# Kernel tuning notes

Hardware: AMD Instinct MI355X
Metric: run time of the kernel (lower is better)

The kernel has to match this reference:

```python
import jax, jax.numpy as jnp
import numpy as np

B, T, C, HD = 4, 4096, 1024, 64  # batch, seq, n_embd, head_dim = n_embd//n_head


def setup_inputs() -> dict:
    key = jax.random.key(0)
    k1, k2, k3, k4 = jax.random.split(key, 4)
    scale = 0.02
    return {
        "x": jax.random.normal(k1, (B, T, C), dtype=jnp.float32),
        "Wq": jax.random.normal(k2, (C, HD), dtype=jnp.float32) * scale,
        "Wk": jax.random.normal(k3, (C, HD), dtype=jnp.float32) * scale,
        "Wv": jax.random.normal(k4, (C, HD), dtype=jnp.float32) * scale,
    }


def reference(x, Wq, Wk, Wv):
    # single-head projections: [B,T,C] @ [C,HD] -> [B,T,HD]
    q = jnp.einsum("btc,ch->bth", x, Wq)
    k = jnp.einsum("btc,ch->bth", x, Wk)
    v = jnp.einsum("btc,ch->bth", x, Wv)
    scale = k.shape[-1] ** -0.5
    # scores: [B,T,T], causal mask via -inf, stable softmax
    alpha = jnp.einsum("bqh,bkh->bqk", q, k) * scale
    t = x.shape[1]
    causal = jnp.tril(jnp.ones((t, t), dtype=bool))
    alpha = jnp.where(causal, alpha, -jnp.inf)
    alpha = jax.nn.softmax(alpha, axis=-1)
    # dropout p=0.0 -> identity
    h = jnp.einsum("bqk,bkh->bqh", alpha, v)
    return h
```

## Files before the change

kernel.cpp:

```cpp
#include <hip/hip_runtime.h>

#define T_SEQ 4096
#define C_DIM 1024
#define HD 64
#define NCH 272

typedef __attribute__((ext_vector_type(8))) __bf16 bf16x8;
typedef __attribute__((ext_vector_type(8))) unsigned short us8;
typedef __attribute__((ext_vector_type(4))) unsigned short us4;
typedef __attribute__((ext_vector_type(4))) float f32x4;
typedef __attribute__((ext_vector_type(16))) float f32x16;

#define QSCALE 0.18033688011112042f

__device__ __forceinline__ unsigned short f2bf(float f) {
    union { float f; unsigned u; } x; x.f = f;
    unsigned r = x.u + 0x7FFFu + ((x.u >> 16) & 1u);
    return (unsigned short)(r >> 16);
}

__device__ __forceinline__ float bf2f(unsigned short u) {
    union { unsigned u; float f; } x; x.u = ((unsigned)u) << 16;
    return x.f;
}

__device__ __forceinline__ us8 cvt8(float4 a, float4 b) {
    union { __bf16 h[8]; us8 v; } u;
    u.h[0] = (__bf16)a.x; u.h[1] = (__bf16)a.y; u.h[2] = (__bf16)a.z; u.h[3] = (__bf16)a.w;
    u.h[4] = (__bf16)b.x; u.h[5] = (__bf16)b.y; u.h[6] = (__bf16)b.z; u.h[7] = (__bf16)b.w;
    return u.v;
}

__device__ __forceinline__ us4 cvt4f(float a, float b, float c, float d) {
    union { __bf16 h[4]; us4 v; } u;
    u.h[0] = (__bf16)a; u.h[1] = (__bf16)b; u.h[2] = (__bf16)c; u.h[3] = (__bf16)d;
    return u.v;
}

__device__ __forceinline__ f32x16 zero16() {
    f32x16 v;
    #pragma unroll
    for (int j = 0; j < 16; ++j) v[j] = 0.f;
    return v;
}

__device__ __forceinline__ int swzs(int idx) {
    return idx ^ ((((idx) >> 6) & 7) << 3);
}

__device__ __forceinline__ int offf(int qt) {
    const int m = qt >> 1;
    return (qt & 1) ? (m + 1) * (m + 1) : m * m + m;
}

__global__ __launch_bounds__(256) void k_wtrans(const float* __restrict__ Wq,
                                                const float* __restrict__ Wk,
                                                const float* __restrict__ Wv,
                                                unsigned short* __restrict__ wt_g) {
    __shared__ unsigned short tile[64][72];
    const int bx = blockIdx.x;
    const int which = bx >> 4;
    const int k0 = (bx & 15) * 64;
    const float* W = (which == 0) ? Wq : ((which == 1) ? Wk : Wv);
    const int t = threadIdx.x;
    {
        const int r = t >> 2, c0 = (t & 3) * 16;
        const float4* src = reinterpret_cast<const float4*>(W + (k0 + r) * HD + c0);
        #pragma unroll
        for (int i = 0; i < 4; ++i) {
            float4 v = src[i];
            tile[r][c0 + 4 * i + 0] = f2bf(v.x);
            tile[r][c0 + 4 * i + 1] = f2bf(v.y);
            tile[r][c0 + 4 * i + 2] = f2bf(v.z);
            tile[r][c0 + 4 * i + 3] = f2bf(v.w);
        }
    }
    __syncthreads();
    {
        const int n = t >> 2, kc0 = (t & 3) * 16;
        alignas(16) unsigned short o[16];
        #pragma unroll
        for (int i = 0; i < 16; ++i) o[i] = tile[kc0 + i][n];
        unsigned short* dst = wt_g + (size_t)(which * 64 + n) * 1024 + k0 + kc0;
        *reinterpret_cast<us8*>(dst)     = *reinterpret_cast<const us8*>(&o[0]);
        *reinterpret_cast<us8*>(dst + 8) = *reinterpret_cast<const us8*>(&o[8]);
    }
}

__global__ __launch_bounds__(256) void k_proj(const float* __restrict__ x,
                                              const unsigned short* __restrict__ wt_g,
                                              unsigned short* __restrict__ qs,
                                              unsigned short* __restrict__ ksb,
                                              unsigned short* __restrict__ vt) {
    __shared__ unsigned short smem[6656];
    unsigned short* xs0 = smem;
    unsigned short* xs1 = smem + 2304;
    const int tid = threadIdx.x;
    const int w = tid >> 6, lane = tid & 63;
    const int l15 = lane & 15, g = lane >> 4;
    const int m0 = blockIdx.x * 32;
    const int sr = tid >> 3, sc0 = (tid & 7) * 8;
    const float* xrow = x + (size_t)(m0 + sr) * C_DIM + sc0;
    const unsigned short* wrow[3];
    #pragma unroll
    for (int mf = 0; mf < 3; ++mf)
        wrow[mf] = wt_g + (size_t)((3 * w + mf) * 16 + l15) * C_DIM + g * 8;

    f32x4 acc[3][2];
    #pragma unroll
    for (int mf = 0; mf < 3; ++mf)
        #pragma unroll
        for (int nf = 0; nf < 2; ++nf)
            acc[mf][nf] = (f32x4){0.f, 0.f, 0.f, 0.f};

    {
        float4 xa = *reinterpret_cast<const float4*>(xrow);
        float4 xb = *reinterpret_cast<const float4*>(xrow + 4);
        *reinterpret_cast<us8*>(xs0 + sr * 72 + sc0) = cvt8(xa, xb);
    }
    float4 p1a = *reinterpret_cast<const float4*>(xrow + 64);
    float4 p1b = *reinterpret_cast<const float4*>(xrow + 68);
    us8 wc[3][2];
    #pragma unroll
    for (int mf = 0; mf < 3; ++mf)
        #pragma unroll
        for (int k2 = 0; k2 < 2; ++k2)
            wc[mf][k2] = *reinterpret_cast<const us8*>(wrow[mf] + k2 * 32);
    __syncthreads();

    for (int kk = 0; kk < 16; ++kk) {
        unsigned short* xcur = (kk & 1) ? xs1 : xs0;
        unsigned short* xnxt = (kk & 1) ? xs0 : xs1;
        float4 p2a, p2b;
        us8 wn[3][2];
        if (kk < 14) {
            p2a = *reinterpret_cast<const float4*>(xrow + (kk + 2) * 64);
            p2b = *reinterpret_cast<const float4*>(xrow + (kk + 2) * 64 + 4);
        }
        if (kk < 15) {
            #pragma unroll
            for (int mf = 0; mf < 3; ++mf)
                #pragma unroll
                for (int k2 = 0; k2 < 2; ++k2)
                    wn[mf][k2] = *reinterpret_cast<const us8*>(wrow[mf] + (kk + 1) * 64 + k2 * 32);
        }
        #pragma unroll
        for (int k2 = 0; k2 < 2; ++k2) {
            bf16x8 bfr[2];
            #pragma unroll
            for (int nf = 0; nf < 2; ++nf)
                bfr[nf] = *reinterpret_cast<const bf16x8*>(xcur + (nf * 16 + l15) * 72 + k2 * 32 + g * 8);
            #pragma unroll
            for (int mf = 0; mf < 3; ++mf) {
                bf16x8 afr = *reinterpret_cast<const bf16x8*>(&wc[mf][k2]);
                #pragma unroll
                for (int nf = 0; nf < 2; ++nf)
                    acc[mf][nf] = __builtin_amdgcn_mfma_f32_16x16x32_bf16(
                        afr, bfr[nf], acc[mf][nf], 0, 0, 0);
            }
        }
        if (kk < 15) {
            *reinterpret_cast<us8*>(xnxt + sr * 72 + sc0) = cvt8(p1a, p1b);
            #pragma unroll
            for (int mf = 0; mf < 3; ++mf)
                #pragma unroll
                for (int k2 = 0; k2 < 2; ++k2)
                    wc[mf][k2] = wn[mf][k2];
        }
        p1a = p2a; p1b = p2b;
        __syncthreads();
    }

    unsigned short* out_lds = smem;
    #pragma unroll
    for (int mf = 0; mf < 3; ++mf) {
        const int Mfr = 3 * w + mf;
        const float s = (Mfr < 4) ? QSCALE : 1.0f;
        #pragma unroll
        for (int nf = 0; nf < 2; ++nf) {
            union { __bf16 h[4]; us4 v; } u;
            #pragma unroll
            for (int r = 0; r < 4; ++r) u.h[r] = (__bf16)(acc[mf][nf][r] * s);
            *reinterpret_cast<us4*>(out_lds + (nf * 16 + l15) * 208 + Mfr * 16 + 4 * g) = u.v;
        }
    }
    __syncthreads();
    {
        const int r = tid >> 3, c = (tid & 7) * 8;
        const size_t gm = (size_t)(m0 + r);
        *reinterpret_cast<us8*>(qs + gm * 64 + c)  = *reinterpret_cast<const us8*>(out_lds + r * 208 + c);
        *reinterpret_cast<us8*>(ksb + gm * 64 + c) = *reinterpret_cast<const us8*>(out_lds + r * 208 + 64 + c);
    }
    {
        const int d = tid >> 2, j0 = (tid & 3) * 8;
        const int b = m0 >> 12, t0 = m0 & 4095;
        alignas(16) unsigned short tmp[8];
        #pragma unroll
        for (int j = 0; j < 8; ++j) tmp[j] = out_lds[(j0 + j) * 208 + 128 + d];
        *reinterpret_cast<us8*>(vt + (size_t)(b * 64 + d) * T_SEQ + t0 + j0) =
            *reinterpret_cast<const us8*>(tmp);
    }
}

__global__ __launch_bounds__(256) void k_attn(const unsigned short* __restrict__ qs,
                                              const unsigned short* __restrict__ ks,
                                              const unsigned short* __restrict__ vt,
                                              unsigned short* __restrict__ Opart,
                                              float* __restrict__ lw,
                                              float* __restrict__ out) {
    __shared__ unsigned short sm[16384];
    const int tid = threadIdx.x;
    const int w = tid >> 6, lane = tid & 63;
    const int l31 = lane & 31, hi = lane >> 5;
    const int batch = blockIdx.y;
    const int i = (NCH - 1) - blockIdx.x;
    int qt = min(31, (int)(2.0f * sqrtf((float)i)));
    while (offf(qt + 1) <= i) ++qt;
    while (offf(qt) > i) --qt;
    const int s = i - offf(qt);
    const int ns = (qt + 2) >> 1;
    const int it0 = s * 4;
    const int it1 = min(it0 + 4, 2 * qt + 2);
    const int qi = qt * 128 + 32 * w + l31;
    const size_t qrow = (size_t)batch * T_SEQ + qi;

    bf16x8 qf[4];
    #pragma unroll
    for (int df = 0; df < 4; ++df)
        qf[df] = *reinterpret_cast<const bf16x8*>(qs + qrow * 64 + df * 16 + hi * 8);

    f32x16 accO0 = zero16(), accO1 = zero16();
    float l_run = 0.f;

    const int sr = tid >> 2, sc0 = (tid & 3) * 16;
    const unsigned short* kbase = ks + ((size_t)batch * T_SEQ + sr) * 64 + sc0;
    const unsigned short* vbase = vt + ((size_t)batch * 64 + sr) * T_SEQ + sc0;

    {
        us8 a0 = *reinterpret_cast<const us8*>(kbase + (size_t)it0 * 4096);
        us8 a1 = *reinterpret_cast<const us8*>(kbase + (size_t)it0 * 4096 + 8);
        us8 b0 = *reinterpret_cast<const us8*>(vbase + it0 * 64);
        us8 b1 = *reinterpret_cast<const us8*>(vbase + it0 * 64 + 8);
        us8 w0, w1;
        #pragma unroll
        for (int j = 0; j < 4; ++j) { w0[j] = b0[j]; w0[4 + j] = b1[j]; w1[j] = b0[4 + j]; w1[4 + j] = b1[4 + j]; }
        const int kd = sr * 64 + sc0, vd = 8192 + sr * 64 + sc0;
        *reinterpret_cast<us8*>(sm + swzs(kd))     = a0;
        *reinterpret_cast<us8*>(sm + swzs(kd + 8)) = a1;
        *reinterpret_cast<us8*>(sm + swzs(vd))     = w0;
        *reinterpret_cast<us8*>(sm + swzs(vd + 8)) = w1;
    }
    __syncthreads();

    for (int it = it0; it < it1; ++it) {
        const int cur = (it - it0) & 1;
        const bool pf = (it + 1 < it1);
        us8 n0, n1, m0, m1;
        if (pf) {
            n0 = *reinterpret_cast<const us8*>(kbase + (size_t)(it + 1) * 4096);
            n1 = *reinterpret_cast<const us8*>(kbase + (size_t)(it + 1) * 4096 + 8);
            m0 = *reinterpret_cast<const us8*>(vbase + (it + 1) * 64);
            m1 = *reinterpret_cast<const us8*>(vbase + (it + 1) * 64 + 8);
        }
        const int kb = cur * 4096;
        const int vb = 8192 + cur * 4096;
        const bool diag = (it >= 2 * qt);

        #pragma unroll
        for (int ksub = 0; ksub < 2; ++ksub) {
            f32x16 sv = zero16();
            __builtin_amdgcn_s_setprio(1);
            #pragma unroll
            for (int df = 0; df < 4; ++df) {
                bf16x8 afr = *reinterpret_cast<const bf16x8*>(
                    sm + swzs(kb + (ksub * 32 + l31) * 64 + df * 16 + hi * 8));
                sv = __builtin_amdgcn_mfma_f32_32x32x16_bf16(afr, qf[df], sv, 0, 0, 0);
            }
            __builtin_amdgcn_s_setprio(0);
            if (diag) {
                #pragma unroll
                for (int rr = 0; rr < 16; ++rr) {
                    const int kidx = it * 64 + ksub * 32 + (rr & 3) + 8 * (rr >> 2) + 4 * hi;
                    if (kidx > qi) sv[rr] = -1e30f;
                }
            }
            f32x16 pv;
            #pragma unroll
            for (int rr = 0; rr < 16; ++rr) {
                const float p = exp2f(sv[rr]);
                l_run += p;
                pv[rr] = p;
            }
            us8 bfr0, bfr1;
            {
                us4 c0 = cvt4f(pv[0], pv[1], pv[2], pv[3]);
                us4 c1 = cvt4f(pv[4], pv[5], pv[6], pv[7]);
                us4 c2 = cvt4f(pv[8], pv[9], pv[10], pv[11]);
                us4 c3 = cvt4f(pv[12], pv[13], pv[14], pv[15]);
                #pragma unroll
                for (int j = 0; j < 4; ++j) {
                    bfr0[j] = c0[j]; bfr0[4 + j] = c1[j];
                    bfr1[j] = c2[j]; bfr1[4 + j] = c3[j];
                }
            }
            __builtin_amdgcn_s_setprio(1);
            {
                bf16x8 a00 = *reinterpret_cast<const bf16x8*>(
                    sm + swzs(vb + l31 * 64 + ksub * 32 + hi * 8));
                bf16x8 a01 = *reinterpret_cast<const bf16x8*>(
                    sm + swzs(vb + l31 * 64 + ksub * 32 + 16 + hi * 8));
                accO0 = __builtin_amdgcn_mfma_f32_32x32x16_bf16(
                    a00, *reinterpret_cast<bf16x8*>(&bfr0), accO0, 0, 0, 0);
                accO0 = __builtin_amdgcn_mfma_f32_32x32x16_bf16(
                    a01, *reinterpret_cast<bf16x8*>(&bfr1), accO0, 0, 0, 0);
                bf16x8 a10 = *reinterpret_cast<const bf16x8*>(
                    sm + swzs(vb + (32 + l31) * 64 + ksub * 32 + hi * 8));
                bf16x8 a11 = *reinterpret_cast<const bf16x8*>(
                    sm + swzs(vb + (32 + l31) * 64 + ksub * 32 + 16 + hi * 8));
                accO1 = __builtin_amdgcn_mfma_f32_32x32x16_bf16(
                    a10, *reinterpret_cast<bf16x8*>(&bfr0), accO1, 0, 0, 0);
                accO1 = __builtin_amdgcn_mfma_f32_32x32x16_bf16(
                    a11, *reinterpret_cast<bf16x8*>(&bfr1), accO1, 0, 0, 0);
            }
            __builtin_amdgcn_s_setprio(0);
        }
        if (pf) {
            us8 w0, w1;
            #pragma unroll
            for (int j = 0; j < 4; ++j) { w0[j] = m0[j]; w0[4 + j] = m1[j]; w1[j] = m0[4 + j]; w1[4 + j] = m1[4 + j]; }
            const int kd = (cur ^ 1) * 4096 + sr * 64 + sc0;
            const int vd = 8192 + (cur ^ 1) * 4096 + sr * 64 + sc0;
            *reinterpret_cast<us8*>(sm + swzs(kd))     = n0;
            *reinterpret_cast<us8*>(sm + swzs(kd + 8)) = n1;
            *reinterpret_cast<us8*>(sm + swzs(vd))     = w0;
            *reinterpret_cast<us8*>(sm + swzs(vd + 8)) = w1;
        }
        __syncthreads();
    }

    l_run += __shfl_xor(l_run, 32, 64);

    if (ns == 1) {
        const float inv = 1.0f / l_run;
        #pragma unroll
        for (int rg = 0; rg < 4; ++rg) {
            const int d0 = 4 * hi + 8 * rg;
            f32x4 o0 = {accO0[4 * rg] * inv, accO0[4 * rg + 1] * inv,
                        accO0[4 * rg + 2] * inv, accO0[4 * rg + 3] * inv};
            f32x4 o1 = {accO1[4 * rg] * inv, accO1[4 * rg + 1] * inv,
                        accO1[4 * rg + 2] * inv, accO1[4 * rg + 3] * inv};
            *reinterpret_cast<f32x4*>(out + qrow * 64 + d0)      = o0;
            *reinterpret_cast<f32x4*>(out + qrow * 64 + 32 + d0) = o1;
        }
    } else {
        const int pb = batch * NCH + i;
        const int q = 32 * w + l31;
        unsigned short* ob = Opart + (size_t)pb * 8192 + q * 64;
        #pragma unroll
        for (int rg = 0; rg < 4; ++rg) {
            const int d0 = 4 * hi + 8 * rg;
            *reinterpret_cast<us4*>(ob + d0) =
                cvt4f(accO0[4 * rg], accO0[4 * rg + 1], accO0[4 * rg + 2], accO0[4 * rg + 3]);
            *reinterpret_cast<us4*>(ob + 32 + d0) =
                cvt4f(accO1[4 * rg], accO1[4 * rg + 1], accO1[4 * rg + 2], accO1[4 * rg + 3]);
        }
        if (hi == 0) lw[(size_t)pb * 128 + q] = l_run;
    }
}

__global__ __launch_bounds__(256) void k_combine(const unsigned short* __restrict__ Opart,
                                                 const float* __restrict__ lw,
                                                 float* __restrict__ out) {
    const int qt = 2 + (blockIdx.x >> 1), half = blockIdx.x & 1;
    const int batch = blockIdx.y;
    const int t = threadIdx.x;
    const int q = half * 64 + (t >> 2), d0 = (t & 3) * 16;
    const int ns = (qt + 2) >> 1;
    const int pb0 = batch * NCH + offf(qt);
    float num[16];
    #pragma unroll
    for (int j = 0; j < 16; ++j) num[j] = 0.f;
    float lsum = 0.f;
    for (int s = 0; s < ns; ++s) {
        const int pb = pb0 + s;
        lsum += lw[(size_t)pb * 128 + q];
        const unsigned short* op = Opart + (size_t)pb * 8192 + q * 64 + d0;
        us8 v0 = *reinterpret_cast<const us8*>(op);
        us8 v1 = *reinterpret_cast<const us8*>(op + 8);
        #pragma unroll
        for (int j = 0; j < 8; ++j) {
            num[j] += bf2f(v0[j]);
            num[8 + j] += bf2f(v1[j]);
        }
    }
    const float inv = 1.f / lsum;
    float* o = out + ((size_t)batch * T_SEQ + qt * 128 + q) * 64 + d0;
    #pragma unroll
    for (int h = 0; h < 4; ++h) {
        f32x4 v = {num[4 * h] * inv, num[4 * h + 1] * inv,
                   num[4 * h + 2] * inv, num[4 * h + 3] * inv};
        *reinterpret_cast<f32x4*>(o + 4 * h) = v;
    }
}

extern "C" void kernel_launch(void* const* d_in, const int* in_sizes, int n_in,
                              void* d_out, int out_size, void* d_ws, size_t ws_size,
                              hipStream_t stream) {
    (void)in_sizes; (void)n_in; (void)out_size; (void)ws_size;
    const float* x  = (const float*)d_in[0];
    const float* Wq = (const float*)d_in[1];
    const float* Wk = (const float*)d_in[2];
    const float* Wv = (const float*)d_in[3];
    float* out = (float*)d_out;
    unsigned short* ws16 = (unsigned short*)d_ws;
    unsigned short* wt_g  = ws16;
    unsigned short* qsb   = ws16 + 196608;
    unsigned short* ksb   = qsb + 1048576;
    unsigned short* vtb   = ksb + 1048576;
    unsigned short* Opart = vtb + 1048576;
    float* lw = (float*)(Opart + 8912896);
    k_wtrans <<<dim3(48),      dim3(256), 0, stream>>>(Wq, Wk, Wv, wt_g);
    k_proj   <<<dim3(512),     dim3(256), 0, stream>>>(x, wt_g, qsb, ksb, vtb);
    k_attn   <<<dim3(NCH, 4),  dim3(256), 0, stream>>>(qsb, ksb, vtb, Opart, lw, out);
    k_combine<<<dim3(60, 4),   dim3(256), 0, stream>>>(Opart, lw, out);
}
```

Baseline: 68.14 us.

## Stage x in 256-wide K groups and split softmax row-sum accumulator

The projection kernel now converts and stages x into LDS in 256-column groups, double-buffered across four outer iterations, instead of 64-column chunks. This cuts the number of block-wide barriers from sixteen to four and prefetches larger batches of global loads. It costs more LDS per block (about 33KB) and more registers for the eight prefetch float4s, which may lower occupancy. Separately, the attention kernel splits the running exp-sum into four independent accumulators to shorten the serial add dependency chain.

```diff
diff --git a/kernel.cpp b/kernel.cpp
--- a/kernel.cpp
+++ b/kernel.cpp
@@ -92,9 +92,7 @@
                                               unsigned short* __restrict__ qs,
                                               unsigned short* __restrict__ ksb,
                                               unsigned short* __restrict__ vt) {
-    __shared__ unsigned short smem[6656];
-    unsigned short* xs0 = smem;
-    unsigned short* xs1 = smem + 2304;
+    __shared__ unsigned short smem[16896];
     const int tid = threadIdx.x;
     const int w = tid >> 6, lane = tid & 63;
     const int l15 = lane & 15, g = lane >> 4;
@@ -113,13 +111,18 @@
         for (int nf = 0; nf < 2; ++nf)
             acc[mf][nf] = (f32x4){0.f, 0.f, 0.f, 0.f};
 
-    {
-        float4 xa = *reinterpret_cast<const float4*>(xrow);
-        float4 xb = *reinterpret_cast<const float4*>(xrow + 4);
-        *reinterpret_cast<us8*>(xs0 + sr * 72 + sc0) = cvt8(xa, xb);
-    }
-    float4 p1a = *reinterpret_cast<const float4*>(xrow + 64);
-    float4 p1b = *reinterpret_cast<const float4*>(xrow + 68);
+    #pragma unroll
+    for (int cg = 0; cg < 4; ++cg) {
+        float4 a = *reinterpret_cast<const float4*>(xrow + cg * 64);
+        float4 b = *reinterpret_cast<const float4*>(xrow + cg * 64 + 4);
+        *reinterpret_cast<us8*>(smem + sr * 264 + cg * 64 + sc0) = cvt8(a, b);
+    }
+    float4 pa[4], pb[4];
+    #pragma unroll
+    for (int cg = 0; cg < 4; ++cg) {
+        pa[cg] = *reinterpret_cast<const float4*>(xrow + 256 + cg * 64);
+        pb[cg] = *reinterpret_cast<const float4*>(xrow + 256 + cg * 64 + 4);
+    }
     us8 wc[3][2];
     #pragma unroll
     for (int mf = 0; mf < 3; ++mf)
@@ -128,46 +131,56 @@
             wc[mf][k2] = *reinterpret_cast<const us8*>(wrow[mf] + k2 * 32);
     __syncthreads();
 
-    for (int kk = 0; kk < 16; ++kk) {
-        unsigned short* xcur = (kk & 1) ? xs1 : xs0;
-        unsigned short* xnxt = (kk & 1) ? xs0 : xs1;
-        float4 p2a, p2b;
-        us8 wn[3][2];
-        if (kk < 14) {
-            p2a = *reinterpret_cast<const float4*>(xrow + (kk + 2) * 64);
-            p2b = *reinterpret_cast<const float4*>(xrow + (kk + 2) * 64 + 4);
-        }
-        if (kk < 15) {
-            #pragma unroll
-            for (int mf = 0; mf < 3; ++mf)
-                #pragma unroll
-                for (int k2 = 0; k2 < 2; ++k2)
-                    wn[mf][k2] = *reinterpret_cast<const us8*>(wrow[mf] + (kk + 1) * 64 + k2 * 32);
-        }
-        #pragma unroll
-        for (int k2 = 0; k2 < 2; ++k2) {
-            bf16x8 bfr[2];
-            #pragma unroll
-            for (int nf = 0; nf < 2; ++nf)
-                bfr[nf] = *reinterpret_cast<const bf16x8*>(xcur + (nf * 16 + l15) * 72 + k2 * 32 + g * 8);
-            #pragma unroll
-            for (int mf = 0; mf < 3; ++mf) {
-                bf16x8 afr = *reinterpret_cast<const bf16x8*>(&wc[mf][k2]);
+    for (int grp = 0; grp < 4; ++grp) {
+        unsigned short* xcur = (grp & 1) ? (smem + 8448) : smem;
+        unsigned short* xnxt = (grp & 1) ? smem : (smem + 8448);
+        #pragma unroll
+        for (int kk2 = 0; kk2 < 4; ++kk2) {
+            const int kk = grp * 4 + kk2;
+            us8 wn[3][2];
+            if (kk < 15) {
+                #pragma unroll
+                for (int mf = 0; mf < 3; ++mf)
+                    #pragma unroll
+                    for (int k2 = 0; k2 < 2; ++k2)
+                        wn[mf][k2] = *reinterpret_cast<const us8*>(wrow[mf] + (kk + 1) * 64 + k2 * 32);
+            }
+            #pragma unroll
+            for (int k2 = 0; k2 < 2; ++k2) {
+                bf16x8 bfr[2];
                 #pragma unroll
                 for (int nf = 0; nf < 2; ++nf)
-                    acc[mf][nf] = __builtin_amdgcn_mfma_f32_16x16x32_bf16(
-                        afr, bfr[nf], acc[mf][nf], 0, 0, 0);
-            }
-        }
-        if (kk < 15) {
-            *reinterpret_cast<us8*>(xnxt + sr * 72 + sc0) = cvt8(p1a, p1b);
-            #pragma unroll
-            for (int mf = 0; mf < 3; ++mf)
-                #pragma unroll
-                for (int k2 = 0; k2 < 2; ++k2)
-                    wc[mf][k2] = wn[mf][k2];
-        }
-        p1a = p2a; p1b = p2b;
+                    bfr[nf] = *reinterpret_cast<const bf16x8*>(
+                        xcur + (nf * 16 + l15) * 264 + kk2 * 64 + k2 * 32 + g * 8);
+                #pragma unroll
+                for (int mf = 0; mf < 3; ++mf) {
+                    bf16x8 afr = *reinterpret_cast<const bf16x8*>(&wc[mf][k2]);
+                    #pragma unroll
+                    for (int nf = 0; nf < 2; ++nf)
+                        acc[mf][nf] = __builtin_amdgcn_mfma_f32_16x16x32_bf16(
+                            afr, bfr[nf], acc[mf][nf], 0, 0, 0);
+                }
+            }
+            if (kk < 15) {
+                #pragma unroll
+                for (int mf = 0; mf < 3; ++mf)
+                    #pragma unroll
+                    for (int k2 = 0; k2 < 2; ++k2)
+                        wc[mf][k2] = wn[mf][k2];
+            }
+        }
+        if (grp < 3) {
+            #pragma unroll
+            for (int cg = 0; cg < 4; ++cg)
+                *reinterpret_cast<us8*>(xnxt + sr * 264 + cg * 64 + sc0) = cvt8(pa[cg], pb[cg]);
+            if (grp < 2) {
+                #pragma unroll
+                for (int cg = 0; cg < 4; ++cg) {
+                    pa[cg] = *reinterpret_cast<const float4*>(xrow + (grp + 2) * 256 + cg * 64);
+                    pb[cg] = *reinterpret_cast<const float4*>(xrow + (grp + 2) * 256 + cg * 64 + 4);
+                }
+            }
+        }
         __syncthreads();
     }
 
@@ -230,7 +243,7 @@
         qf[df] = *reinterpret_cast<const bf16x8*>(qs + qrow * 64 + df * 16 + hi * 8);
 
     f32x16 accO0 = zero16(), accO1 = zero16();
-    float l_run = 0.f;
+    float lp0 = 0.f, lp1 = 0.f, lp2 = 0.f, lp3 = 0.f;
 
     const int sr = tid >> 2, sc0 = (tid & 3) * 16;
     const unsigned short* kbase = ks + ((size_t)batch * T_SEQ + sr) * 64 + sc0;
@@ -286,10 +299,13 @@
             }
             f32x16 pv;
             #pragma unroll
-            for (int rr = 0; rr < 16; ++rr) {
-                const float p = exp2f(sv[rr]);
-                l_run += p;
-                pv[rr] = p;
+            for (int rr = 0; rr < 16; ++rr) pv[rr] = exp2f(sv[rr]);
+            #pragma unroll
+            for (int rr = 0; rr < 4; ++rr) {
+                lp0 += pv[4 * rr + 0];
+                lp1 += pv[4 * rr + 1];
+                lp2 += pv[4 * rr + 2];
+                lp3 += pv[4 * rr + 3];
             }
             us8 bfr0, bfr1;
             {
@@ -338,6 +354,7 @@
         __syncthreads();
     }
 
+    float l_run = (lp0 + lp1) + (lp2 + lp3);
     l_run += __shfl_xor(l_run, 32, 64);
 
     if (ns == 1) {
```

Result: slower. 73.79 us (+8.3%).

## Double projection tile to 64 rows with 8 waves and split attention row-sum accumulators

Applied to the files above, without the earlier changes.

The projection kernel now uses 512-thread blocks covering 64 rows. Each weight fragment loaded into registers is reused by two waves working on different row halves, which halves the number of blocks and the redundant weight traffic. The x prefetch distance drops from two k-steps to one, which exposes more load latency. In the attention kernel the softmax row-sum is accumulated into four independent partial sums to break the serial add dependency chain.

```diff
diff --git a/kernel.cpp b/kernel.cpp
--- a/kernel.cpp
+++ b/kernel.cpp
@@ -87,24 +87,25 @@
     }
 }
 
-__global__ __launch_bounds__(256) void k_proj(const float* __restrict__ x,
+__global__ __launch_bounds__(512) void k_proj(const float* __restrict__ x,
                                               const unsigned short* __restrict__ wt_g,
                                               unsigned short* __restrict__ qs,
                                               unsigned short* __restrict__ ksb,
                                               unsigned short* __restrict__ vt) {
-    __shared__ unsigned short smem[6656];
+    __shared__ unsigned short smem[13312];
     unsigned short* xs0 = smem;
-    unsigned short* xs1 = smem + 2304;
+    unsigned short* xs1 = smem + 4608;
     const int tid = threadIdx.x;
     const int w = tid >> 6, lane = tid & 63;
     const int l15 = lane & 15, g = lane >> 4;
-    const int m0 = blockIdx.x * 32;
+    const int wm = w & 1, wn = w >> 1;
+    const int m0 = blockIdx.x * 64;
     const int sr = tid >> 3, sc0 = (tid & 7) * 8;
     const float* xrow = x + (size_t)(m0 + sr) * C_DIM + sc0;
     const unsigned short* wrow[3];
     #pragma unroll
     for (int mf = 0; mf < 3; ++mf)
-        wrow[mf] = wt_g + (size_t)((3 * w + mf) * 16 + l15) * C_DIM + g * 8;
+        wrow[mf] = wt_g + (size_t)((3 * wn + mf) * 16 + l15) * C_DIM + g * 8;
 
     f32x4 acc[3][2];
     #pragma unroll
@@ -118,8 +119,6 @@
         float4 xb = *reinterpret_cast<const float4*>(xrow + 4);
         *reinterpret_cast<us8*>(xs0 + sr * 72 + sc0) = cvt8(xa, xb);
     }
-    float4 p1a = *reinterpret_cast<const float4*>(xrow + 64);
-    float4 p1b = *reinterpret_cast<const float4*>(xrow + 68);
     us8 wc[3][2];
     #pragma unroll
     for (int mf = 0; mf < 3; ++mf)
@@ -131,25 +130,25 @@
     for (int kk = 0; kk < 16; ++kk) {
         unsigned short* xcur = (kk & 1) ? xs1 : xs0;
         unsigned short* xnxt = (kk & 1) ? xs0 : xs1;
-        float4 p2a, p2b;
-        us8 wn[3][2];
-        if (kk < 14) {
-            p2a = *reinterpret_cast<const float4*>(xrow + (kk + 2) * 64);
-            p2b = *reinterpret_cast<const float4*>(xrow + (kk + 2) * 64 + 4);
-        }
-        if (kk < 15) {
+        const bool pf = (kk < 15);
+        float4 na, nb;
+        us8 wn2[3][2];
+        if (pf) {
+            na = *reinterpret_cast<const float4*>(xrow + (kk + 1) * 64);
+            nb = *reinterpret_cast<const float4*>(xrow + (kk + 1) * 64 + 4);
             #pragma unroll
             for (int mf = 0; mf < 3; ++mf)
                 #pragma unroll
                 for (int k2 = 0; k2 < 2; ++k2)
-                    wn[mf][k2] = *reinterpret_cast<const us8*>(wrow[mf] + (kk + 1) * 64 + k2 * 32);
+                    wn2[mf][k2] = *reinterpret_cast<const us8*>(wrow[mf] + (kk + 1) * 64 + k2 * 32);
         }
         #pragma unroll
         for (int k2 = 0; k2 < 2; ++k2) {
             bf16x8 bfr[2];
             #pragma unroll
             for (int nf = 0; nf < 2; ++nf)
-                bfr[nf] = *reinterpret_cast<const bf16x8*>(xcur + (nf * 16 + l15) * 72 + k2 * 32 + g * 8);
+                bfr[nf] = *reinterpret_cast<const bf16x8*>(
+                    xcur + (wm * 32 + nf * 16 + l15) * 72 + k2 * 32 + g * 8);
             #pragma unroll
             for (int mf = 0; mf < 3; ++mf) {
                 bf16x8 afr = *reinterpret_cast<const bf16x8*>(&wc[mf][k2]);
@@ -159,29 +158,29 @@
                         afr, bfr[nf], acc[mf][nf], 0, 0, 0);
             }
         }
-        if (kk < 15) {
-            *reinterpret_cast<us8*>(xnxt + sr * 72 + sc0) = cvt8(p1a, p1b);
+        if (pf) {
+            *reinterpret_cast<us8*>(xnxt + sr * 72 + sc0) = cvt8(na, nb);
             #pragma unroll
             for (int mf = 0; mf < 3; ++mf)
                 #pragma unroll
                 for (int k2 = 0; k2 < 2; ++k2)
-                    wc[mf][k2] = wn[mf][k2];
-        }
-        p1a = p2a; p1b = p2b;
+                    wc[mf][k2] = wn2[mf][k2];
+        }
         __syncthreads();
     }
 
     unsigned short* out_lds = smem;
     #pragma unroll
     for (int mf = 0; mf < 3; ++mf) {
-        const int Mfr = 3 * w + mf;
+        const int Mfr = 3 * wn + mf;
         const float s = (Mfr < 4) ? QSCALE : 1.0f;
         #pragma unroll
         for (int nf = 0; nf < 2; ++nf) {
             union { __bf16 h[4]; us4 v; } u;
             #pragma unroll
             for (int r = 0; r < 4; ++r) u.h[r] = (__bf16)(acc[mf][nf][r] * s);
-            *reinterpret_cast<us4*>(out_lds + (nf * 16 + l15) * 208 + Mfr * 16 + 4 * g) = u.v;
+            *reinterpret_cast<us4*>(
+                out_lds + (wm * 32 + nf * 16 + l15) * 208 + Mfr * 16 + 4 * g) = u.v;
         }
     }
     __syncthreads();
@@ -192,7 +191,7 @@
         *reinterpret_cast<us8*>(ksb + gm * 64 + c) = *reinterpret_cast<const us8*>(out_lds + r * 208 + 64 + c);
     }
     {
-        const int d = tid >> 2, j0 = (tid & 3) * 8;
+        const int d = tid >> 3, j0 = (tid & 7) * 8;
         const int b = m0 >> 12, t0 = m0 & 4095;
         alignas(16) unsigned short tmp[8];
         #pragma unroll
@@ -230,7 +229,7 @@
         qf[df] = *reinterpret_cast<const bf16x8*>(qs + qrow * 64 + df * 16 + hi * 8);
 
     f32x16 accO0 = zero16(), accO1 = zero16();
-    float l_run = 0.f;
+    float lp0 = 0.f, lp1 = 0.f, lp2 = 0.f, lp3 = 0.f;
 
     const int sr = tid >> 2, sc0 = (tid & 3) * 16;
     const unsigned short* kbase = ks + ((size_t)batch * T_SEQ + sr) * 64 + sc0;
@@ -286,10 +285,13 @@
             }
             f32x16 pv;
             #pragma unroll
-            for (int rr = 0; rr < 16; ++rr) {
-                const float p = exp2f(sv[rr]);
-                l_run += p;
-                pv[rr] = p;
+            for (int rr = 0; rr < 16; ++rr) pv[rr] = exp2f(sv[rr]);
+            #pragma unroll
+            for (int rr = 0; rr < 4; ++rr) {
+                lp0 += pv[4 * rr + 0];
+                lp1 += pv[4 * rr + 1];
+                lp2 += pv[4 * rr + 2];
+                lp3 += pv[4 * rr + 3];
             }
             us8 bfr0, bfr1;
             {
@@ -338,6 +340,7 @@
         __syncthreads();
     }
 
+    float l_run = (lp0 + lp1) + (lp2 + lp3);
     l_run += __shfl_xor(l_run, 32, 64);
 
     if (ns == 1) {
@@ -420,7 +423,7 @@
     unsigned short* Opart = vtb + 1048576;
     float* lw = (float*)(Opart + 8912896);
     k_wtrans <<<dim3(48),      dim3(256), 0, stream>>>(Wq, Wk, Wv, wt_g);
-    k_proj   <<<dim3(512),     dim3(256), 0, stream>>>(x, wt_g, qsb, ksb, vtb);
+    k_proj   <<<dim3(256),     dim3(512), 0, stream>>>(x, wt_g, qsb, ksb, vtb);
     k_attn   <<<dim3(NCH, 4),  dim3(256), 0, stream>>>(qsb, ksb, vtb, Opart, lw, out);
     k_combine<<<dim3(60, 4),   dim3(256), 0, stream>>>(Opart, lw, out);
 }
```

After: 71.28 us. 4.6% more time.
